# Kernel tuning notes

Hardware: AMD Instinct MI355X
Metric: run time of the kernel (lower is better)

Reference implementation:

```python
import jax, jax.numpy as jnp
import numpy as np

DIM = 1024
HEADS = 16
HEAD_DIM = DIM // HEADS
HIDDEN = 4 * DIM
EPS = 1e-5


def layer_norm(x, g, b):
    mu = jnp.mean(x, axis=-1, keepdims=True)
    var = jnp.mean(jnp.square(x - mu), axis=-1, keepdims=True)
    return (x - mu) * jax.lax.rsqrt(var + EPS) * g + b


def fast_gelu(x):
    # Ascend fast_gelu == x * sigmoid(1.702 * x)
    return x * jax.nn.sigmoid(1.702 * x)


def setup_inputs() -> dict:
    key = jax.random.key(0)
    ks = jax.random.split(key, 12)
    B, N, C = 16, 577, DIM
    s_in = 1.0 / np.sqrt(DIM)
    s_hid = 1.0 / np.sqrt(HIDDEN)
    return {
        "x": jax.random.normal(ks[0], (B * N, C), jnp.float32),
        "norm1_g": jnp.ones((C,), jnp.float32),
        "norm1_b": jnp.zeros((C,), jnp.float32),
        "Wq": jax.random.normal(ks[1], (C, C), jnp.float32) * s_in,
        "Wk": jax.random.normal(ks[2], (C, C), jnp.float32) * s_in,
        "Wv": jax.random.normal(ks[3], (C, C), jnp.float32) * s_in,
        "Wp": jax.random.normal(ks[4], (C, C), jnp.float32) * s_in,
        "bp": jnp.zeros((C,), jnp.float32),
        "norm2_g": jnp.ones((C,), jnp.float32),
        "norm2_b": jnp.zeros((C,), jnp.float32),
        "W1": jax.random.normal(ks[5], (HIDDEN, C), jnp.float32) * s_in,
        "b1": jnp.zeros((HIDDEN,), jnp.float32),
        "W2": jax.random.normal(ks[6], (C, HIDDEN), jnp.float32) * s_hid,
        "b2": jnp.zeros((C,), jnp.float32),
        "B": B,
        "N": N,
        "C": C,
    }


def reference(x, norm1_g, norm1_b, Wq, Wk, Wv, Wp, bp, norm2_g, norm2_b, W1, b1, W2, b2, B, N, C):
    scale = HEAD_DIM ** -0.5

    h = layer_norm(x, norm1_g, norm1_b)          # [B*N, C]
    # qkv projections (qkv_bias=False), reshape to [B, H, N, D]
    def split_heads(y):
        return y.reshape(B, N, HEADS, HEAD_DIM).transpose(0, 2, 1, 3)

    q = split_heads(h @ Wq.T)
    k = split_heads(h @ Wk.T)
    v = split_heads(h @ Wv.T)

    attn = jnp.einsum('bhqd,bhkd->bhqk', q, k) * scale
    attn = jax.nn.softmax(attn, axis=-1)
    o = jnp.einsum('bhqk,bhkd->bhqd', attn, v)   # [B, H, N, D]
    o = o.transpose(0, 2, 1, 3).reshape(B * N, C)
    y = o @ Wp.T + bp                            # attention output proj

    x = x + y                                    # residual 1 (drop_path=0)
    h2 = layer_norm(x, norm2_g, norm2_b)
    m = fast_gelu(h2 @ W1.T + b1) @ W2.T + b2    # MLP (drop=0)
    return x + m                                 # residual 2
```

## Files before the change

kernel.cpp:

```cpp
#include <hip/hip_runtime.h>

typedef short  short8  __attribute__((ext_vector_type(8)));
typedef float  float4v __attribute__((ext_vector_type(4)));

#define DIM      1024
#define HEADS    16
#define HEAD_DIM 64
#define HIDDEN   4096
#define BATCH    16
#define SEQ      577
#define M_ROWS   (BATCH*SEQ)
#define NPAD2    640
#define QKVLD    3072
#define LOG2E    1.4426950408889634f

static __device__ __forceinline__ unsigned short f2bf(float f) {
  unsigned int u = __float_as_uint(f);
  u += 0x7FFFu + ((u >> 16) & 1u);
  return (unsigned short)(u >> 16);
}
static __device__ __forceinline__ void gload_lds16(const void* g, void* l) {
  __builtin_amdgcn_global_load_lds(
      (const __attribute__((address_space(1))) void*)g,
      (__attribute__((address_space(3))) void*)l, 16, 0, 0);
}
static __device__ __forceinline__ int xcd_chunk(int w, int nwg) {
  int xcd = w & 7, rest = w >> 3;
  int q = nwg >> 3, r = nwg & 7;
  int base = xcd < r ? xcd * (q + 1) : r * (q + 1) + (xcd - r) * q;
  return base + rest;
}

__global__ __launch_bounds__(256) void convert_all_kernel(
    const float* __restrict__ Wq, const float* __restrict__ Wk,
    const float* __restrict__ Wv, const float* __restrict__ Wp,
    const float* __restrict__ W1, const float* __restrict__ W2,
    unsigned short* __restrict__ wqkv, unsigned short* __restrict__ wp,
    unsigned short* __restrict__ w1, unsigned short* __restrict__ w2) {
  const int S = DIM * DIM / 4;
  int i = blockIdx.x * 256 + threadIdx.x;
  const float* src; unsigned short* dst; int rel;
  if (i < 4 * S) {
    if (i < S)        { src = Wq; dst = wqkv;               rel = i; }
    else if (i < 2*S) { src = Wk; dst = wqkv + DIM * DIM;   rel = i - S; }
    else if (i < 3*S) { src = Wv; dst = wqkv + 2*DIM*DIM;   rel = i - 2*S; }
    else              { src = Wp; dst = wp;                 rel = i - 3*S; }
  } else if (i < 8*S) { src = W1; dst = w1;                 rel = i - 4*S; }
  else                { src = W2; dst = w2;                 rel = i - 8*S; }
  float4 v = ((const float4*)src)[rel];
  union { unsigned short s[4]; uint2 u; } p;
  p.s[0] = f2bf(v.x); p.s[1] = f2bf(v.y); p.s[2] = f2bf(v.z); p.s[3] = f2bf(v.w);
  ((uint2*)dst)[rel] = p.u;
}

__global__ __launch_bounds__(256) void ln_kernel(
    const float* __restrict__ x, const float* __restrict__ g,
    const float* __restrict__ b, unsigned short* __restrict__ out) {
  int row = blockIdx.x, tid = threadIdx.x;
  const float* xr = x + (long long)row * DIM;
  float4 v = *(const float4*)(xr + tid * 4);
  float s1 = v.x + v.y + v.z + v.w;
  float s2 = v.x*v.x + v.y*v.y + v.z*v.z + v.w*v.w;
  #pragma unroll
  for (int o = 32; o; o >>= 1) { s1 += __shfl_xor(s1, o); s2 += __shfl_xor(s2, o); }
  __shared__ float a1[4], a2[4];
  int wid = tid >> 6, lane = tid & 63;
  if (lane == 0) { a1[wid] = s1; a2[wid] = s2; }
  __syncthreads();
  s1 = a1[0] + a1[1] + a1[2] + a1[3];
  s2 = a2[0] + a2[1] + a2[2] + a2[3];
  float mean = s1 * (1.f / DIM);
  float var  = s2 * (1.f / DIM) - mean * mean;
  float rstd = rsqrtf(var + 1e-5f);
  float4 gv = *(const float4*)(g + tid * 4);
  float4 bv = *(const float4*)(b + tid * 4);
  union { unsigned short s[4]; uint2 u; } p;
  p.s[0] = f2bf((v.x - mean) * rstd * gv.x + bv.x);
  p.s[1] = f2bf((v.y - mean) * rstd * gv.y + bv.y);
  p.s[2] = f2bf((v.z - mean) * rstd * gv.z + bv.z);
  p.s[3] = f2bf((v.w - mean) * rstd * gv.w + bv.w);
  *(uint2*)(out + (long long)row * DIM + tid * 4) = p.u;
}

__global__ __launch_bounds__(256) void transpose_v_kernel(
    const unsigned short* __restrict__ v, unsigned short* __restrict__ vt) {
  int nt0 = blockIdx.x * 64;
  int bh = blockIdx.y;
  int b = bh >> 4, h = bh & 15;
  __shared__ unsigned short T[64][72];
  int tid = threadIdx.x;
  int r = tid >> 3;
  int c = tid & 7;
  #pragma unroll
  for (int p = 0; p < 2; p++) {
    int row = p * 32 + r;
    int n = nt0 + row;
    uint4 val = (uint4){0u, 0u, 0u, 0u};
    if (n < SEQ)
      val = *(const uint4*)(v + ((long long)(b * SEQ + n)) * QKVLD + h * HEAD_DIM + c * 8);
    *(uint4*)&T[row][c * 8] = val;
  }
  __syncthreads();
  #pragma unroll
  for (int p = 0; p < 2; p++) {
    int d = p * 32 + (tid >> 3);
    union { unsigned short s[8]; uint4 u; } o;
    #pragma unroll
    for (int i = 0; i < 8; i++) o.s[i] = T[c * 8 + i][d];
    *(uint4*)(vt + ((long long)bh * HEAD_DIM + d) * NPAD2 + nt0 + c * 8) = o.u;
  }
}

template <bool MASK>
static __device__ __forceinline__ void attn_tile(
    const unsigned short* Ks, const unsigned short* Vs, unsigned short* Ps,
    const short8 (&af)[2][2], float4v (&oacc)[2][4], float4v (&sumacc)[2],
    int quad, int l16, int wid) {
  const float CE = 0.125f * LOG2E;

  short8 bfr[4][2];
  #pragma unroll
  for (int j = 0; j < 4; j++) {
    int r = j * 16 + l16;
    #pragma unroll
    for (int ks = 0; ks < 2; ks++)
      bfr[j][ks] = *(const short8*)(Ks + r * 64 + ((ks * 4 + quad) ^ (l16 & 7)) * 8);
  }

  float4v sacc[2][4];
  #pragma unroll
  for (int i = 0; i < 2; i++)
    #pragma unroll
    for (int j = 0; j < 4; j++) sacc[i][j] = (float4v){0.f, 0.f, 0.f, 0.f};
  #pragma unroll
  for (int i = 0; i < 2; i++)
    #pragma unroll
    for (int j = 0; j < 4; j++)
      #pragma unroll
      for (int ks = 0; ks < 2; ks++)
        sacc[i][j] = __builtin_amdgcn_mfma_f32_16x16x32_bf16(af[i][ks], bfr[j][ks], sacc[i][j], 0, 0, 0);

  #pragma unroll
  for (int i = 0; i < 2; i++) {
    #pragma unroll
    for (int reg = 0; reg < 4; reg++) {
      int prow = wid * 32 + i * 16 + quad * 4 + reg;
      #pragma unroll
      for (int j = 0; j < 4; j++) {
        float pv;
        if constexpr (MASK) {
          pv = (j == 0 && l16 == 0) ? __builtin_amdgcn_exp2f(sacc[i][j][reg] * CE) : 0.f;
        } else {
          pv = __builtin_amdgcn_exp2f(sacc[i][j][reg] * CE);
        }
        int pcol = j * 16 + l16;
        Ps[prow * 64 + (((pcol >> 3) ^ (prow & 7)) * 8) + (pcol & 7)] = f2bf(pv);
      }
    }
  }

  short8 paf[2][2], vbf[4][2];
  #pragma unroll
  for (int i = 0; i < 2; i++) {
    int r = wid * 32 + i * 16 + l16;
    #pragma unroll
    for (int kk = 0; kk < 2; kk++)
      paf[i][kk] = *(const short8*)(Ps + r * 64 + ((kk * 4 + quad) ^ (l16 & 7)) * 8);
  }
  #pragma unroll
  for (int j = 0; j < 4; j++) {
    int r = j * 16 + l16;
    #pragma unroll
    for (int kk = 0; kk < 2; kk++)
      vbf[j][kk] = *(const short8*)(Vs + r * 64 + ((kk * 4 + quad) ^ (l16 & 7)) * 8);
  }
  const short ov = (short)0x3F80;
  const short8 ones = (short8){ov, ov, ov, ov, ov, ov, ov, ov};
  #pragma unroll
  for (int i = 0; i < 2; i++) {
    #pragma unroll
    for (int kk = 0; kk < 2; kk++) {
      #pragma unroll
      for (int j = 0; j < 4; j++)
        oacc[i][j] = __builtin_amdgcn_mfma_f32_16x16x32_bf16(paf[i][kk], vbf[j][kk], oacc[i][j], 0, 0, 0);
      sumacc[i] = __builtin_amdgcn_mfma_f32_16x16x32_bf16(paf[i][kk], ones, sumacc[i], 0, 0, 0);
    }
  }
}

__global__ __launch_bounds__(256, 3) void flash_attn_kernel(
    const unsigned short* __restrict__ q,
    const unsigned short* __restrict__ k,
    const unsigned short* __restrict__ vt,
    unsigned short* __restrict__ o) {
  int w = blockIdx.y * 5 + blockIdx.x;
  int id = xcd_chunk(w, 5 * 256);
  int qt = id % 5;
  int bh = id / 5;
  int b = bh >> 4, h = bh & 15;
  int q0 = qt * 128;
  int tid = threadIdx.x, lane = tid & 63, wid = tid >> 6;
  int quad = lane >> 4, l16 = lane & 15;
  long long rowbase = (long long)b * SEQ;

  __shared__ __align__(16) unsigned short SM[24576];
  unsigned short* Ps = SM + 16384;

  int sr = wid * 16 + (lane >> 3);
  int scc = (lane & 7) ^ (sr & 7);
  const unsigned short* kbase = k + (rowbase + sr) * QKVLD + h * HEAD_DIM + scc * 8;
  const unsigned short* kbase2 = k + (rowbase + sr + 8) * QKVLD + h * HEAD_DIM + (((lane & 7) ^ ((sr + 8) & 7)) * 8);
  const unsigned short* vbase = vt + ((long long)bh * HEAD_DIM + sr) * NPAD2 + scc * 8;
  const unsigned short* vbase2 = vt + ((long long)bh * HEAD_DIM + sr + 8) * NPAD2 + (((lane & 7) ^ ((sr + 8) & 7)) * 8);

  auto stageKV = [&](int sel, int kt) {
    unsigned short* Ks_ = SM + sel * 8192;
    unsigned short* Vs_ = Ks_ + 4096;
    long long koff = (long long)kt * 64 * QKVLD;
    long long koff2 = koff;
    if (kt == 9) {
      koff  -= (long long)((kt * 64 + sr)     - (SEQ - 1) > 0 ? (kt * 64 + sr)     - (SEQ - 1) : 0) * QKVLD;
      koff2 -= (long long)((kt * 64 + sr + 8) - (SEQ - 1) > 0 ? (kt * 64 + sr + 8) - (SEQ - 1) : 0) * QKVLD;
    }
    gload_lds16(kbase  + koff,  Ks_ + sr * 64 - (lane >> 3) * 64);
    gload_lds16(kbase2 + koff2, Ks_ + (sr + 8) * 64 - (lane >> 3) * 64);
    gload_lds16(vbase  + kt * 64, Vs_ + sr * 64 - (lane >> 3) * 64);
    gload_lds16(vbase2 + kt * 64, Vs_ + (sr + 8) * 64 - (lane >> 3) * 64);
  };

  short8 af[2][2];
  #pragma unroll
  for (int i = 0; i < 2; i++) {
    int gr = q0 + wid * 32 + i * 16 + l16;
    if (gr > SEQ - 1) gr = SEQ - 1;
    const unsigned short* qr = q + (rowbase + gr) * QKVLD + h * HEAD_DIM;
    #pragma unroll
    for (int ks = 0; ks < 2; ks++)
      af[i][ks] = *(const short8*)(qr + (ks * 4 + quad) * 8);
  }

  float4v oacc[2][4];
  float4v sumacc[2];
  #pragma unroll
  for (int i = 0; i < 2; i++) {
    sumacc[i] = (float4v){0.f, 0.f, 0.f, 0.f};
    #pragma unroll
    for (int j = 0; j < 4; j++) oacc[i][j] = (float4v){0.f, 0.f, 0.f, 0.f};
  }

  stageKV(0, 0);

  for (int kt = 0; kt < 10; kt++) {
    int cur = kt & 1;
    if (kt < 9) {
      stageKV(cur ^ 1, kt + 1);
      asm volatile("s_waitcnt vmcnt(4)" ::: "memory");
    } else {
      asm volatile("s_waitcnt vmcnt(0)" ::: "memory");
    }
    __builtin_amdgcn_s_barrier();
    const unsigned short* Ks_ = SM + cur * 8192;
    const unsigned short* Vs_ = Ks_ + 4096;
    if (kt < 9) attn_tile<false>(Ks_, Vs_, Ps, af, oacc, sumacc, quad, l16, wid);
    else        attn_tile<true >(Ks_, Vs_, Ps, af, oacc, sumacc, quad, l16, wid);
    asm volatile("" ::: "memory");
    __builtin_amdgcn_s_barrier();
  }

  #pragma unroll
  for (int i = 0; i < 2; i++) {
    #pragma unroll
    for (int reg = 0; reg < 4; reg++) {
      int grow = q0 + wid * 32 + i * 16 + quad * 4 + reg;
      if (grow >= SEQ) continue;
      float inv = 1.f / sumacc[i][reg];
      #pragma unroll
      for (int j = 0; j < 4; j++) {
        int d = j * 16 + l16;
        o[(rowbase + grow) * DIM + h * HEAD_DIM + d] = f2bf(oacc[i][j][reg] * inv);
      }
    }
  }
}

enum { EPI_BF16 = 0, EPI_BIAS_RES_F32 = 2, EPI_BIAS_GELU_BF16 = 3 };

template <int EPI>
__global__ __launch_bounds__(256, 2) void gemm_nt(
    const unsigned short* __restrict__ A, int lda,
    const unsigned short* __restrict__ B, int ldb,
    void* __restrict__ Cout, int ldc,
    const float* __restrict__ bias, const float* __restrict__ res,
    int M, int N, int K) {
  int mt = gridDim.x, nt = gridDim.y;
  int nwg = mt * nt;
  int id = xcd_chunk(blockIdx.y * mt + blockIdx.x, nwg);
  int band  = id / (8 * nt);
  int rem   = id - band * 8 * nt;
  int mrem  = mt - band * 8;
  int bandh = mrem < 8 ? mrem : 8;
  int lm = rem % bandh;
  int nb = rem / bandh;
  int m0 = (band * 8 + lm) * 128, n0 = nb * 128;

  int tid = threadIdx.x;
  int lane = tid & 63, wid = tid >> 6;
  int wm = wid >> 1, wn = wid & 1;
  int quad = lane >> 4, l16 = lane & 15;

  __shared__ __align__(16) char SMEM[65536];

  float4v acc[4][4];
  #pragma unroll
  for (int i = 0; i < 4; i++)
    #pragma unroll
    for (int j = 0; j < 4; j++) acc[i][j] = (float4v){0.f, 0.f, 0.f, 0.f};

  int lr8 = lane >> 3;
  int sc  = ((lane & 7) ^ lr8) * 8;

  const unsigned short* pA[4];
  const unsigned short* pB[4];
  #pragma unroll
  for (int p = 0; p < 4; p++) {
    int ra = wid * 32 + p * 8;
    int gr = m0 + ra + lr8; if (gr > M - 1) gr = M - 1;
    pA[p] = A + (long long)gr * lda + sc;
    int gn = n0 + ra + lr8; if (gn > N - 1) gn = N - 1;
    pB[p] = B + (long long)gn * ldb + sc;
  }

  auto stage = [&](int sel, int k0) {
    unsigned short* As_ = (unsigned short*)SMEM + sel * (2 * 128 * 64);
    unsigned short* Bs_ = As_ + 128 * 64;
    #pragma unroll
    for (int p = 0; p < 4; p++) {
      int ra = wid * 32 + p * 8;
      gload_lds16(pA[p] + k0, As_ + ra * 64);
      gload_lds16(pB[p] + k0, Bs_ + ra * 64);
    }
  };

  int T = K >> 6;
  stage(0, 0);

  for (int t = 0; t < T; t++) {
    int cur = t & 1;
    if (t + 1 < T) {
      stage(cur ^ 1, (t + 1) << 6);
      asm volatile("s_waitcnt vmcnt(8)" ::: "memory");
    } else {
      asm volatile("s_waitcnt vmcnt(0)" ::: "memory");
    }
    __builtin_amdgcn_s_barrier();
    const unsigned short* As_ = (const unsigned short*)SMEM + cur * (2 * 128 * 64);
    const unsigned short* Bs_ = As_ + 128 * 64;
    #pragma unroll
    for (int ks = 0; ks < 2; ks++) {
      short8 af[4], bfr[4];
      #pragma unroll
      for (int i = 0; i < 4; i++)
        af[i]  = *(const short8*)(As_ + (wm * 64 + i * 16 + l16) * 64 + (((ks * 4 + quad) ^ (l16 & 7)) * 8));
      #pragma unroll
      for (int j = 0; j < 4; j++)
        bfr[j] = *(const short8*)(Bs_ + (wn * 64 + j * 16 + l16) * 64 + (((ks * 4 + quad) ^ (l16 & 7)) * 8));
      #pragma unroll
      for (int i = 0; i < 4; i++)
        #pragma unroll
        for (int j = 0; j < 4; j++)
          acc[i][j] = __builtin_amdgcn_mfma_f32_16x16x32_bf16(af[i], bfr[j], acc[i][j], 0, 0, 0);
    }
    asm volatile("" ::: "memory");
    __builtin_amdgcn_s_barrier();
  }

  float* cs = (float*)SMEM + wid * (16 * 68);
  int erow = lane >> 2;
  int eq   = lane & 3;

  #pragma unroll
  for (int i = 0; i < 4; i++) {
    #pragma unroll
    for (int j = 0; j < 4; j++)
      #pragma unroll
      for (int r = 0; r < 4; r++)
        cs[(quad * 4 + r) * 68 + j * 16 + l16] = acc[i][j][r];
    int grow = m0 + wm * 64 + i * 16 + erow;
    bool rowok = grow < M;

    if constexpr (EPI == EPI_BIAS_RES_F32) {
      #pragma unroll
      for (int t = 0; t < 4; t++) {
        int colb = t * 16 + eq * 4;
        int gcol = n0 + wn * 64 + colb;
        if (!rowok || gcol >= N) continue;
        float4 vv = *(const float4*)&cs[erow * 68 + colb];
        float4 bb = *(const float4*)&bias[gcol];
        const float4 rr = *(const float4*)&res[(long long)grow * ldc + gcol];
        vv.x += bb.x + rr.x; vv.y += bb.y + rr.y;
        vv.z += bb.z + rr.z; vv.w += bb.w + rr.w;
        *(float4*)((float*)Cout + (long long)grow * ldc + gcol) = vv;
      }
    } else {
      #pragma unroll
      for (int h = 0; h < 2; h++) {
        int colb = h * 32 + eq * 8;
        int gcol = n0 + wn * 64 + colb;
        if (!rowok || gcol >= N) continue;
        float4 a0 = *(const float4*)&cs[erow * 68 + colb];
        float4 a1 = *(const float4*)&cs[erow * 68 + colb + 4];
        float vs[8] = {a0.x, a0.y, a0.z, a0.w, a1.x, a1.y, a1.z, a1.w};
        if constexpr (EPI == EPI_BIAS_GELU_BF16) {
          float4 b0 = *(const float4*)&bias[gcol];
          float4 b1 = *(const float4*)&bias[gcol + 4];
          float bs[8] = {b0.x, b0.y, b0.z, b0.w, b1.x, b1.y, b1.z, b1.w};
          #pragma unroll
          for (int e = 0; e < 8; e++) {
            float tt = vs[e] + bs[e];
            float ex = __builtin_amdgcn_exp2f(tt * -2.4554669595930156f);
            vs[e] = tt / (1.f + ex);
          }
        }
        union { unsigned short s[8]; uint4 u; } p;
        #pragma unroll
        for (int e = 0; e < 8; e++) p.s[e] = f2bf(vs[e]);
        *(uint4*)((unsigned short*)Cout + (long long)grow * ldc + gcol) = p.u;
      }
    }
  }
}

extern "C" void kernel_launch(void* const* d_in, const int* in_sizes, int n_in,
                              void* d_out, int out_size, void* d_ws, size_t ws_size,
                              hipStream_t stream) {
  const float* x   = (const float*)d_in[0];
  const float* g1  = (const float*)d_in[1];
  const float* be1 = (const float*)d_in[2];
  const float* Wq  = (const float*)d_in[3];
  const float* Wk  = (const float*)d_in[4];
  const float* Wv  = (const float*)d_in[5];
  const float* Wp  = (const float*)d_in[6];
  const float* bp  = (const float*)d_in[7];
  const float* g2  = (const float*)d_in[8];
  const float* be2 = (const float*)d_in[9];
  const float* W1  = (const float*)d_in[10];
  const float* b1  = (const float*)d_in[11];
  const float* W2  = (const float*)d_in[12];
  const float* b2  = (const float*)d_in[13];
  float* out = (float*)d_out;

  char* ws = (char*)d_ws;
  size_t off = 0;
  auto alloc = [&](size_t bytes) {
    size_t r = off; off += (bytes + 255) & ~(size_t)255; return r;
  };
  unsigned short* wqkv_bf = (unsigned short*)(ws + alloc((size_t)3 * DIM * DIM * 2));
  unsigned short* wp_bf   = (unsigned short*)(ws + alloc((size_t)DIM * DIM * 2));
  unsigned short* w1_bf   = (unsigned short*)(ws + alloc((size_t)HIDDEN * DIM * 2));
  unsigned short* w2_bf   = (unsigned short*)(ws + alloc((size_t)HIDDEN * DIM * 2));
  unsigned short* h_bf    = (unsigned short*)(ws + alloc((size_t)M_ROWS * DIM * 2));
  unsigned short* qkv_bf  = (unsigned short*)(ws + alloc((size_t)M_ROWS * QKVLD * 2));
  unsigned short* vt_bf   = (unsigned short*)(ws + alloc((size_t)256 * HEAD_DIM * NPAD2 * 2));

  unsigned short* o_bf  = h_bf;
  unsigned short* h2_bf = h_bf;
  unsigned short* u_bf  = qkv_bf;
  float*          x1    = out;

  convert_all_kernel<<<12 * (DIM * DIM / 4) / 256, 256, 0, stream>>>(
      Wq, Wk, Wv, Wp, W1, W2, wqkv_bf, wp_bf, w1_bf, w2_bf);

  ln_kernel<<<M_ROWS, 256, 0, stream>>>(x, g1, be1, h_bf);

  gemm_nt<EPI_BF16><<<dim3(73, 24), 256, 0, stream>>>(h_bf, DIM, wqkv_bf, DIM,
      qkv_bf, QKVLD, nullptr, nullptr, M_ROWS, 3 * DIM, DIM);

  transpose_v_kernel<<<dim3(10, 256), 256, 0, stream>>>(qkv_bf + 2 * DIM, vt_bf);

  flash_attn_kernel<<<dim3(5, 256), 256, 0, stream>>>(
      qkv_bf, qkv_bf + DIM, vt_bf, o_bf);

  gemm_nt<EPI_BIAS_RES_F32><<<dim3(73, 8), 256, 0, stream>>>(o_bf, DIM, wp_bf, DIM,
      x1, DIM, bp, x, M_ROWS, DIM, DIM);

  ln_kernel<<<M_ROWS, 256, 0, stream>>>(x1, g2, be2, h2_bf);

  gemm_nt<EPI_BIAS_GELU_BF16><<<dim3(73, 32), 256, 0, stream>>>(h2_bf, DIM, w1_bf, DIM,
      u_bf, HIDDEN, b1, nullptr, M_ROWS, HIDDEN, DIM);

  gemm_nt<EPI_BIAS_RES_F32><<<dim3(73, 8), 256, 0, stream>>>(u_bf, HIDDEN, w2_bf, HIDDEN,
      out, DIM, b2, x1, M_ROWS, DIM, HIDDEN);
}
```

Before: 532.0 us.

## Drop GEMM double buffering to halve LDS and raise occupancy to four blocks

Replaces the double-buffered async global-to-LDS pipeline in the NT GEMM with a single 32KB buffer and plain load-sync-compute-sync loop, and raises launch bounds to 4 blocks per CU. The goal is to hide memory latency through more resident waves instead of software prefetch. This exposes load latency within each block and tightens the register budget, which may cause spills with the 64-float accumulator.

```diff
diff --git a/kernel.cpp b/kernel.cpp
--- a/kernel.cpp
+++ b/kernel.cpp
@@ -286,7 +286,7 @@
 enum { EPI_BF16 = 0, EPI_BIAS_RES_F32 = 2, EPI_BIAS_GELU_BF16 = 3 };
 
 template <int EPI>
-__global__ __launch_bounds__(256, 2) void gemm_nt(
+__global__ __launch_bounds__(256, 4) void gemm_nt(
     const unsigned short* __restrict__ A, int lda,
     const unsigned short* __restrict__ B, int ldb,
     void* __restrict__ Cout, int ldc,
@@ -308,7 +308,9 @@
   int wm = wid >> 1, wn = wid & 1;
   int quad = lane >> 4, l16 = lane & 15;
 
-  __shared__ __align__(16) char SMEM[65536];
+  __shared__ __align__(16) char SMEM[32768];
+  unsigned short* As = (unsigned short*)SMEM;
+  unsigned short* Bs = As + 128 * 64;
 
   float4v acc[4][4];
   #pragma unroll
@@ -330,48 +332,30 @@
     pB[p] = B + (long long)gn * ldb + sc;
   }
 
-  auto stage = [&](int sel, int k0) {
-    unsigned short* As_ = (unsigned short*)SMEM + sel * (2 * 128 * 64);
-    unsigned short* Bs_ = As_ + 128 * 64;
+  for (int k0 = 0; k0 < K; k0 += 64) {
     #pragma unroll
     for (int p = 0; p < 4; p++) {
       int ra = wid * 32 + p * 8;
-      gload_lds16(pA[p] + k0, As_ + ra * 64);
-      gload_lds16(pB[p] + k0, Bs_ + ra * 64);
-    }
-  };
-
-  int T = K >> 6;
-  stage(0, 0);
-
-  for (int t = 0; t < T; t++) {
-    int cur = t & 1;
-    if (t + 1 < T) {
-      stage(cur ^ 1, (t + 1) << 6);
-      asm volatile("s_waitcnt vmcnt(8)" ::: "memory");
-    } else {
-      asm volatile("s_waitcnt vmcnt(0)" ::: "memory");
-    }
-    __builtin_amdgcn_s_barrier();
-    const unsigned short* As_ = (const unsigned short*)SMEM + cur * (2 * 128 * 64);
-    const unsigned short* Bs_ = As_ + 128 * 64;
+      gload_lds16(pA[p] + k0, As + ra * 64);
+      gload_lds16(pB[p] + k0, Bs + ra * 64);
+    }
+    __syncthreads();
     #pragma unroll
     for (int ks = 0; ks < 2; ks++) {
       short8 af[4], bfr[4];
       #pragma unroll
       for (int i = 0; i < 4; i++)
-        af[i]  = *(const short8*)(As_ + (wm * 64 + i * 16 + l16) * 64 + (((ks * 4 + quad) ^ (l16 & 7)) * 8));
+        af[i]  = *(const short8*)(As + (wm * 64 + i * 16 + l16) * 64 + (((ks * 4 + quad) ^ (l16 & 7)) * 8));
       #pragma unroll
       for (int j = 0; j < 4; j++)
-        bfr[j] = *(const short8*)(Bs_ + (wn * 64 + j * 16 + l16) * 64 + (((ks * 4 + quad) ^ (l16 & 7)) * 8));
+        bfr[j] = *(const short8*)(Bs + (wn * 64 + j * 16 + l16) * 64 + (((ks * 4 + quad) ^ (l16 & 7)) * 8));
       #pragma unroll
       for (int i = 0; i < 4; i++)
         #pragma unroll
         for (int j = 0; j < 4; j++)
           acc[i][j] = __builtin_amdgcn_mfma_f32_16x16x32_bf16(af[i], bfr[j], acc[i][j], 0, 0, 0);
     }
-    asm volatile("" ::: "memory");
-    __builtin_amdgcn_s_barrier();
+    __syncthreads();
   }
 
   float* cs = (float*)SMEM + wid * (16 * 68);
```

Measured after the change: 502.7 us (median of 2 runs). -5.5%, faster.
